# Optimization experiments

Hardware: AMD Instinct MI355X
Metric: run time of the kernel (lower is better)

Reference implementation:

```python
import jax, jax.numpy as jnp
import numpy as np

HEADS = 16
DIM_HEAD = 64
LN_EPS = 1e-5


def setup_inputs() -> dict:
    key = jax.random.key(0)
    ks = jax.random.split(key, 4)
    b, n, dim = 2, 2048, 1024
    inner = HEADS * DIM_HEAD
    x = jax.random.normal(ks[0], (b, n, dim), dtype=jnp.float32)
    gamma = jnp.ones((dim,), dtype=jnp.float32)
    beta = jnp.zeros((dim,), dtype=jnp.float32)
    w_qkv = jax.random.normal(ks[1], (dim, 3 * inner), dtype=jnp.float32) * (dim ** -0.5)
    w_out = jax.random.normal(ks[2], (inner, dim), dtype=jnp.float32) * (inner ** -0.5)
    b_out = jnp.zeros((dim,), dtype=jnp.float32)
    return {"x": x, "gamma": gamma, "beta": beta, "w_qkv": w_qkv, "w_out": w_out, "b_out": b_out}


def reference(x, gamma, beta, w_qkv, w_out, b_out):
    b, n, dim = x.shape
    h, d = HEADS, DIM_HEAD
    scale = d ** -0.5
    # LayerNorm
    mu = jnp.mean(x, axis=-1, keepdims=True)
    var = jnp.mean(jnp.square(x - mu), axis=-1, keepdims=True)
    xn = (x - mu) * jax.lax.rsqrt(var + LN_EPS) * gamma + beta
    # QKV projection (no bias)
    qkv = xn @ w_qkv  # [b, n, 3*h*d]
    q, k, v = jnp.split(qkv, 3, axis=-1)
    split_heads = lambda t: t.reshape(b, n, h, d).transpose(0, 2, 1, 3)  # [b, h, n, d]
    q, k, v = split_heads(q), split_heads(k), split_heads(v)
    q = q * scale
    sim = jnp.einsum('bhid,bhjd->bhij', q, k)  # full O(n^2) score matrix
    attn = jax.nn.softmax(sim, axis=-1)
    out = jnp.einsum('bhij,bhjd->bhid', attn, v)
    out = out.transpose(0, 2, 1, 3).reshape(b, n, h * d)
    return out @ w_out + b_out
```

## Files before the change

kernel.cpp:

```cpp
#include <hip/hip_runtime.h>
#include <hip/hip_bf16.h>

#define HEADS 16
#define DH 64
#define DIM 1024
#define SEQ 2048
#define BATCH 2
#define ROWS (BATCH*SEQ)
#define NQKV (3*DIM)
#define NKVT (SEQ/64)
#define NSPLIT 2
#define QSCALE 0.18033688011112042f
#define NBH (BATCH*HEADS)
#define NQROWS (NBH*SEQ)

typedef __attribute__((ext_vector_type(8))) short bf16x8;
typedef __attribute__((ext_vector_type(4))) float f32x4;
typedef __attribute__((ext_vector_type(16))) float f32x16;
typedef __attribute__((ext_vector_type(4))) unsigned u32x4;
typedef __hip_bfloat16 bf16;

static __device__ __forceinline__ bf16 f2bf(float v){ return __float2bfloat16(v); }

static __device__ __forceinline__ unsigned cvtpk(float a, float b){
  unsigned r;
  asm("v_cvt_pk_bf16_f32 %0, %1, %2" : "=v"(r) : "v"(a), "v"(b));
  return r;
}

static __device__ __forceinline__ void gload16(const void* g, void* lds){
  __builtin_amdgcn_global_load_lds((const __attribute__((address_space(1))) void*)g,
                                   (__attribute__((address_space(3))) void*)lds, 16, 0, 0);
}

__global__ __launch_bounds__(256) void ln_kernel(const float* __restrict__ x,
    const float* __restrict__ gamma, const float* __restrict__ beta,
    bf16* __restrict__ xn)
{
  int row = blockIdx.x;
  int tid = threadIdx.x;
  float4 v = ((const float4*)(x + (size_t)row*DIM))[tid];
  float s  = v.x+v.y+v.z+v.w;
  float ss = v.x*v.x+v.y*v.y+v.z*v.z+v.w*v.w;
  #pragma unroll
  for (int m=1;m<64;m<<=1){ s += __shfl_xor(s,m); ss += __shfl_xor(ss,m); }
  __shared__ float red[8];
  int wid = tid>>6;
  if ((tid&63)==0){ red[wid]=s; red[4+wid]=ss; }
  __syncthreads();
  s  = red[0]+red[1]+red[2]+red[3];
  ss = red[4]+red[5]+red[6]+red[7];
  float mu  = s*(1.0f/DIM);
  float var = ss*(1.0f/DIM) - mu*mu;
  float inv = rsqrtf(var + 1e-5f);
  float4 g  = ((const float4*)gamma)[tid];
  float4 bb = ((const float4*)beta)[tid];
  __align__(8) bf16 o[4];
  o[0]=f2bf((v.x-mu)*inv*g.x+bb.x);
  o[1]=f2bf((v.y-mu)*inv*g.y+bb.y);
  o[2]=f2bf((v.z-mu)*inv*g.z+bb.z);
  o[3]=f2bf((v.w-mu)*inv*g.w+bb.w);
  *(uint2*)&xn[(size_t)row*DIM + tid*4] = *(const uint2*)o;
}

__global__ __launch_bounds__(256) void transpose_cast(const float* __restrict__ in,
    bf16* __restrict__ out, int R, int C)
{
  __shared__ __align__(16) bf16 t[64][72];
  int c0 = blockIdx.x*64, r0 = blockIdx.y*64;
  int tid = threadIdx.x;
  int row = tid>>2;
  int cq  = (tid&3)*16;
  #pragma unroll
  for (int j=0;j<4;j++){
    float4 v = *(const float4*)&in[(size_t)(r0+row)*C + c0 + cq + j*4];
    t[cq+j*4+0][row] = f2bf(v.x);
    t[cq+j*4+1][row] = f2bf(v.y);
    t[cq+j*4+2][row] = f2bf(v.z);
    t[cq+j*4+3][row] = f2bf(v.w);
  }
  __syncthreads();
  int c = tid>>2; int rq = (tid&3)*16;
  uint4 u0 = *(const uint4*)&t[c][rq];
  uint4 u1 = *(const uint4*)&t[c][rq+8];
  *(uint4*)&out[(size_t)(c0+c)*R + r0 + rq]     = u0;
  *(uint4*)&out[(size_t)(c0+c)*R + r0 + rq + 8] = u1;
}

template<int BM>
__global__ __launch_bounds__(256) void gemm_bt(
    const bf16* __restrict__ A, const bf16* __restrict__ Bt, int K, int mode,
    bf16* __restrict__ qb, bf16* __restrict__ kb, bf16* __restrict__ vtb,
    float* __restrict__ outf, const float* __restrict__ bias)
{
  constexpr int MT = (BM == 128) ? 4 : 2;
  __shared__ __align__(16) bf16 aL[2][BM*32];
  __shared__ __align__(16) bf16 bL[2][128*32];
  int tid = threadIdx.x;
  int w = tid>>6, l = tid&63;
  int lr = l&15, lh = l>>4;
  int wr = w>>1, wc = w&1;
  int by = blockIdx.y, bx = blockIdx.x;
  const bf16* Ab = A  + (size_t)(by*BM)*K;
  const bf16* Bb = Bt + (size_t)(bx*128)*K;
  int srow = w*32 + (l>>2);
  int scol = ((l&3)*8) ^ (((l>>2)&3)<<3);
  int frsw = (lr&3)<<3;
  int nt = K/32;

  f32x4 acc[MT][4] = {};

  auto STAGE = [&](int buf, int k0){
    if constexpr (BM == 128){
      gload16(Ab + (size_t)(srow   )*K + k0 + scol, &aL[buf][w*1024      ]);
      gload16(Ab + (size_t)(srow+16)*K + k0 + scol, &aL[buf][w*1024 + 512]);
    } else {
      gload16(Ab + (size_t)(tid>>2 )*K + k0 + scol, &aL[buf][w*512       ]);
    }
    gload16(Bb + (size_t)(srow   )*K + k0 + scol, &bL[buf][w*1024      ]);
    gload16(Bb + (size_t)(srow+16)*K + k0 + scol, &bL[buf][w*1024 + 512]);
  };

  STAGE(0, 0);
  for (int t=0; t<nt; t++){
    int cur = t&1;
    __syncthreads();
    if (t+1 < nt) STAGE(cur^1, (t+1)*32);
    bf16x8 af[MT], bfr[4];
    #pragma unroll
    for (int m=0;m<MT;m++)
      af[m]  = *(const bf16x8*)&aL[cur][(wr*(MT*16) + m*16 + lr)*32 + ((lh*8) ^ frsw)];
    #pragma unroll
    for (int n=0;n<4;n++)
      bfr[n] = *(const bf16x8*)&bL[cur][(wc*64 + n*16 + lr)*32 + ((lh*8) ^ frsw)];
    #pragma unroll
    for (int m=0;m<MT;m++)
      #pragma unroll
      for (int n=0;n<4;n++)
        acc[m][n] = __builtin_amdgcn_mfma_f32_16x16x32_bf16(af[m], bfr[n], acc[m][n], 0,0,0);
  }
  int rb = by*BM + wr*(MT*16), cb = bx*128 + wc*64;
  if (mode == 1){
    #pragma unroll
    for (int m=0;m<MT;m++)
      #pragma unroll
      for (int n=0;n<4;n++)
        #pragma unroll
        for (int reg=0;reg<4;reg++){
          int r = rb + m*16 + lh*4 + reg;
          int c = cb + n*16 + lr;
          outf[(size_t)r*DIM + c] = acc[m][n][reg] + bias[c];
        }
  } else if (bx < 8){
    int b = rb >> 11;
    int nn0 = rb & 2047;
    #pragma unroll
    for (int m=0;m<MT;m++)
      #pragma unroll
      for (int n=0;n<4;n++)
        #pragma unroll
        for (int reg=0;reg<4;reg++){
          int nn = nn0 + m*16 + lh*4 + reg;
          int c  = cb + n*16 + lr;
          int hh = c >> 6, dd = c & 63;
          qb[((size_t)(b*HEADS + hh)*SEQ + nn)*DH + dd] = f2bf(acc[m][n][reg]*QSCALE);
        }
  } else if (bx < 16){
    int b = rb >> 11;
    int kvt = (rb & 2047) >> 6;
    int hh0 = ((cb - 1024) >> 6);
    #pragma unroll
    for (int m=0;m<MT;m++)
      #pragma unroll
      for (int reg=0;reg<4;reg++){
        int kvi = m*16 + lh*4 + reg;
        int sw  = (kvi&7)<<3;
        #pragma unroll
        for (int n=0;n<4;n++){
          int dd = n*16 + lr;
          kb[((size_t)(b*HEADS + hh0)*NKVT + kvt)*4096 + kvi*64 + (dd ^ sw)] = f2bf(acc[m][n][reg]);
        }
      }
  } else {
    __syncthreads();
    bf16* tl = (w < 2 ? (bf16*)aL : (bf16*)bL) + (w&1)*4096;
    int b   = rb >> 11;
    int kvt = (rb & 2047) >> 6;
    int hh  = (cb - 2048) >> 6;
    #pragma unroll
    for (int n=0;n<4;n++){
      int dd = n*16 + lr;
      int sw = (dd&7)<<3;
      #pragma unroll
      for (int m=0;m<MT;m++)
        #pragma unroll
        for (int reg=0;reg<4;reg++)
          tl[dd*64 + ((m*16 + lh*4 + reg) ^ sw)] = f2bf(acc[m][n][reg]);
    }
    __syncthreads();
    size_t gb = ((size_t)(b*HEADS + hh)*NKVT + kvt)*4096;
    #pragma unroll
    for (int j=0;j<8;j++)
      *(uint4*)&vtb[gb + j*512 + l*8] = *(const uint4*)&tl[j*512 + l*8];
  }
}

__global__ __launch_bounds__(256,4) void attn_part(
    const bf16* __restrict__ qb, const bf16* __restrict__ kb,
    const bf16* __restrict__ vtb,
    float* __restrict__ Opart, float* __restrict__ Mpart, float* __restrict__ Spart)
{
  __shared__ __align__(16) bf16 Kl[2][4096];
  __shared__ __align__(16) bf16 Vl[2][4096];
  int tid = threadIdx.x;
  int w = tid>>6, l = tid&63;
  int q5 = l & 31;
  int hi = l >> 5;
  int swz = (q5&7)<<3;
  int bh = blockIdx.y;
  int sp = blockIdx.z;
  int ts = sp*16, te = ts+16;
  const bf16* Q  = qb  + (size_t)bh*SEQ*DH;
  const bf16* Kt = kb  + (size_t)bh*NKVT*4096;
  const bf16* Vt = vtb + (size_t)bh*NKVT*4096;
  int q0w = blockIdx.x*128 + w*32;

  int co[4];
  #pragma unroll
  for (int st=0;st<4;st++) co[st] = (st*16 + hi*8) ^ swz;
  int r0 = q5*64, r1 = r0 + 2048;

  bf16x8 qf[4];
  #pragma unroll
  for (int st=0;st<4;st++)
    qf[st] = *(const bf16x8*)&Q[(size_t)(q0w + q5)*DH + st*16 + hi*8];

  bf16x8 vone;
  #pragma unroll
  for (int i=0;i<8;i++) vone[i] = (short)0x3f80;

  f32x16 o0 = {}, o1 = {}, osum = {};
  float mrun = -3e38f;

  {
    const bf16* ks = Kt + (size_t)ts*4096;
    const bf16* vs = Vt + (size_t)ts*4096;
    gload16(ks + w*1024       + l*8, &Kl[0][w*1024      ]);
    gload16(ks + w*1024 + 512 + l*8, &Kl[0][w*1024 + 512]);
    gload16(vs + w*1024       + l*8, &Vl[0][w*1024      ]);
    gload16(vs + w*1024 + 512 + l*8, &Vl[0][w*1024 + 512]);
  }

  for (int t=ts; t<te; t++){
    int cur = (t-ts)&1;
    __syncthreads();
    if (t+1 < te){
      const bf16* ks = Kt + (size_t)(t+1)*4096;
      const bf16* vs = Vt + (size_t)(t+1)*4096;
      gload16(ks + w*1024       + l*8, &Kl[cur^1][w*1024      ]);
      gload16(ks + w*1024 + 512 + l*8, &Kl[cur^1][w*1024 + 512]);
      gload16(vs + w*1024       + l*8, &Vl[cur^1][w*1024      ]);
      gload16(vs + w*1024 + 512 + l*8, &Vl[cur^1][w*1024 + 512]);
    }
    f32x16 s0 = {}, s1 = {};
    __builtin_amdgcn_s_setprio(1);
    #pragma unroll
    for (int st=0;st<4;st++){
      bf16x8 kf0 = *(const bf16x8*)&Kl[cur][r0 + co[st]];
      bf16x8 kf1 = *(const bf16x8*)&Kl[cur][r1 + co[st]];
      s0 = __builtin_amdgcn_mfma_f32_32x32x16_bf16(kf0, qf[st], s0, 0,0,0);
      s1 = __builtin_amdgcn_mfma_f32_32x32x16_bf16(kf1, qf[st], s1, 0,0,0);
    }
    __builtin_amdgcn_s_setprio(0);
    float pm = -3e38f;
    #pragma unroll
    for (int r=0;r<16;r++) pm = fmaxf(pm, fmaxf(s0[r], s1[r]));
    pm = fmaxf(pm, __shfl_xor(pm, 32));
    if (__any(pm > mrun + 8.f)){
      float mn = fmaxf(mrun, pm);
      float sc = __builtin_amdgcn_exp2f(mrun - mn);
      mrun = mn;
      #pragma unroll
      for (int reg=0;reg<16;reg++){
        float scr = __shfl(sc, (l & 32) | ((reg&3) + 8*(reg>>2) + 4*hi));
        o0[reg] *= scr;
        o1[reg] *= scr;
        osum[reg] *= scr;
      }
    }
    #pragma unroll
    for (int r=0;r<16;r++){
      s0[r] = __builtin_amdgcn_exp2f(s0[r] - mrun);
      s1[r] = __builtin_amdgcn_exp2f(s1[r] - mrun);
    }
    #define PV_STEP(SV, SGN, KVS)                                                    \
    {                                                                                \
      unsigned Aw = cvtpk(SV[SGN+0], SV[SGN+1]);                                     \
      unsigned Bw = cvtpk(SV[SGN+2], SV[SGN+3]);                                     \
      unsigned Cw = cvtpk(SV[SGN+4], SV[SGN+5]);                                     \
      unsigned Dw = cvtpk(SV[SGN+6], SV[SGN+7]);                                     \
      asm volatile("v_permlane32_swap_b32 %0, %1" : "+v"(Aw), "+v"(Cw));             \
      asm volatile("v_permlane32_swap_b32 %0, %1" : "+v"(Bw), "+v"(Dw));             \
      u32x4 pw = {Aw, Bw, Cw, Dw};                                                   \
      bf16x8 pa = *(const bf16x8*)&pw;                                               \
      bf16x8 vf0 = *(const bf16x8*)&Vl[cur][r0 + co[KVS]];                           \
      bf16x8 vf1 = *(const bf16x8*)&Vl[cur][r1 + co[KVS]];                           \
      __builtin_amdgcn_s_setprio(1);                                                 \
      o0 = __builtin_amdgcn_mfma_f32_32x32x16_bf16(pa, vf0, o0, 0,0,0);              \
      o1 = __builtin_amdgcn_mfma_f32_32x32x16_bf16(pa, vf1, o1, 0,0,0);              \
      osum = __builtin_amdgcn_mfma_f32_32x32x16_bf16(pa, vone, osum, 0,0,0);         \
      __builtin_amdgcn_s_setprio(0);                                                 \
    }
    PV_STEP(s0, 0, 0)
    PV_STEP(s0, 8, 1)
    PV_STEP(s1, 0, 2)
    PV_STEP(s1, 8, 3)
    #undef PV_STEP
  }
  size_t rbase = ((size_t)sp*NBH + bh)*SEQ;
  #pragma unroll
  for (int reg=0;reg<16;reg++){
    int q = q0w + (reg&3) + 8*(reg>>2) + 4*hi;
    Opart[(rbase + q)*64 + q5]      = o0[reg];
    Opart[(rbase + q)*64 + 32 + q5] = o1[reg];
  }
  if (l < 32)
    Mpart[rbase + q0w + l] = mrun;
  if (q5 == 0){
    #pragma unroll
    for (int reg=0;reg<16;reg++){
      int q = q0w + (reg&3) + 8*(reg>>2) + 4*hi;
      Spart[rbase + q] = osum[reg];
    }
  }
}

__global__ __launch_bounds__(256) void attn_merge(
    const float* __restrict__ Opart, const float* __restrict__ Mpart,
    const float* __restrict__ Spart, bf16* __restrict__ ao)
{
  int r = blockIdx.x*4 + (threadIdx.x>>6);
  int d = threadIdx.x & 63;
  float m0 = Mpart[r], m1 = Mpart[NQROWS + r];
  float m  = fmaxf(m0, m1);
  float c0 = exp2f(m0 - m), c1 = exp2f(m1 - m);
  float denom = Spart[r]*c0 + Spart[NQROWS + r]*c1;
  float v = Opart[(size_t)r*64 + d]*c0
          + Opart[((size_t)NQROWS + r)*64 + d]*c1;
  int bh = r >> 11, q = r & 2047;
  int b = bh >> 4, h = bh & 15;
  ao[((size_t)(b*SEQ + q))*DIM + h*DH + d] = f2bf(v / denom);
}

extern "C" void kernel_launch(void* const* d_in, const int* in_sizes, int n_in,
                              void* d_out, int out_size, void* d_ws, size_t ws_size,
                              hipStream_t stream)
{
  const float* x     = (const float*)d_in[0];
  const float* gamma = (const float*)d_in[1];
  const float* beta  = (const float*)d_in[2];
  const float* w_qkv = (const float*)d_in[3];
  const float* w_out = (const float*)d_in[4];
  const float* b_out = (const float*)d_in[5];
  float* out = (float*)d_out;

  bf16* ws  = (bf16*)d_ws;
  bf16* xn  = ws;
  bf16* wqt = xn  + (size_t)ROWS*DIM;
  bf16* wot = wqt + (size_t)NQKV*DIM;
  bf16* qb  = wot + (size_t)DIM*DIM;
  bf16* kb  = qb  + (size_t)NBH*SEQ*DH;
  bf16* vtb = kb  + (size_t)NBH*SEQ*DH;
  bf16* ao  = vtb + (size_t)NBH*SEQ*DH;
  float* Opart = (float*)(ao + (size_t)ROWS*DIM);
  float* Mpart = Opart + (size_t)NSPLIT*NQROWS*DH;
  float* Spart = Mpart + (size_t)NSPLIT*NQROWS;

  ln_kernel<<<dim3(ROWS), dim3(256), 0, stream>>>(x, gamma, beta, xn);
  transpose_cast<<<dim3(NQKV/64, DIM/64), dim3(256), 0, stream>>>(w_qkv, wqt, DIM, NQKV);
  transpose_cast<<<dim3(DIM/64,  DIM/64), dim3(256), 0, stream>>>(w_out, wot, DIM, DIM);
  gemm_bt<128><<<dim3(NQKV/128, ROWS/128), dim3(256), 0, stream>>>(
      xn, wqt, DIM, 0, qb, kb, vtb, (float*)nullptr, (const float*)nullptr);
  attn_part<<<dim3(SEQ/128, NBH, NSPLIT), dim3(256), 0, stream>>>(
      qb, kb, vtb, Opart, Mpart, Spart);
  attn_merge<<<dim3(NQROWS/4), dim3(256), 0, stream>>>(Opart, Mpart, Spart, ao);
  gemm_bt<64><<<dim3(DIM/128, ROWS/64), dim3(256), 0, stream>>>(
      ao, wot, DIM, 1, (bf16*)nullptr, (bf16*)nullptr, (bf16*)nullptr, out, b_out);
}
```

Baseline: 133.3 us.

## Triple-buffer GEMM LDS staging and store attention partials in bf16

```diff
diff --git a/kernel.cpp b/kernel.cpp
--- a/kernel.cpp
+++ b/kernel.cpp
@@ -94,8 +94,8 @@
     float* __restrict__ outf, const float* __restrict__ bias)
 {
   constexpr int MT = (BM == 128) ? 4 : 2;
-  __shared__ __align__(16) bf16 aL[2][BM*32];
-  __shared__ __align__(16) bf16 bL[2][128*32];
+  __shared__ __align__(16) bf16 aL[3][BM*32];
+  __shared__ __align__(16) bf16 bL[3][128*32];
   int tid = threadIdx.x;
   int w = tid>>6, l = tid&63;
   int lr = l&15, lh = l>>4;
@@ -121,24 +121,39 @@
     gload16(Bb + (size_t)(srow+16)*K + k0 + scol, &bL[buf][w*1024 + 512]);
   };
 
-  STAGE(0, 0);
-  for (int t=0; t<nt; t++){
-    int cur = t&1;
-    __syncthreads();
-    if (t+1 < nt) STAGE(cur^1, (t+1)*32);
+  auto COMPUTE = [&](int buf){
     bf16x8 af[MT], bfr[4];
     #pragma unroll
     for (int m=0;m<MT;m++)
-      af[m]  = *(const bf16x8*)&aL[cur][(wr*(MT*16) + m*16 + lr)*32 + ((lh*8) ^ frsw)];
+      af[m]  = *(const bf16x8*)&aL[buf][(wr*(MT*16) + m*16 + lr)*32 + ((lh*8) ^ frsw)];
     #pragma unroll
     for (int n=0;n<4;n++)
-      bfr[n] = *(const bf16x8*)&bL[cur][(wc*64 + n*16 + lr)*32 + ((lh*8) ^ frsw)];
+      bfr[n] = *(const bf16x8*)&bL[buf][(wc*64 + n*16 + lr)*32 + ((lh*8) ^ frsw)];
     #pragma unroll
     for (int m=0;m<MT;m++)
       #pragma unroll
       for (int n=0;n<4;n++)
         acc[m][n] = __builtin_amdgcn_mfma_f32_16x16x32_bf16(af[m], bfr[n], acc[m][n], 0,0,0);
-  }
+  };
+
+  STAGE(0, 0);
+  STAGE(1, 32);
+  int cur = 0;
+  for (int t=0; t<nt-1; t++){
+    if constexpr (BM == 128) asm volatile("s_waitcnt vmcnt(4)" ::: "memory");
+    else                     asm volatile("s_waitcnt vmcnt(3)" ::: "memory");
+    __builtin_amdgcn_s_barrier();
+    __builtin_amdgcn_sched_barrier(0);
+    int s2 = cur + 2; if (s2 >= 3) s2 -= 3;
+    if (t+2 < nt) STAGE(s2, (t+2)*32);
+    COMPUTE(cur);
+    cur = (cur == 2) ? 0 : cur + 1;
+  }
+  asm volatile("s_waitcnt vmcnt(0)" ::: "memory");
+  __builtin_amdgcn_s_barrier();
+  __builtin_amdgcn_sched_barrier(0);
+  COMPUTE(cur);
+
   int rb = by*BM + wr*(MT*16), cb = bx*128 + wc*64;
   if (mode == 1){
     #pragma unroll
@@ -208,7 +223,7 @@
 __global__ __launch_bounds__(256,4) void attn_part(
     const bf16* __restrict__ qb, const bf16* __restrict__ kb,
     const bf16* __restrict__ vtb,
-    float* __restrict__ Opart, float* __restrict__ Mpart, float* __restrict__ Spart)
+    bf16* __restrict__ Opart, float* __restrict__ Mpart, float* __restrict__ Spart)
 {
   __shared__ __align__(16) bf16 Kl[2][4096];
   __shared__ __align__(16) bf16 Vl[2][4096];
@@ -321,8 +336,8 @@
   #pragma unroll
   for (int reg=0;reg<16;reg++){
     int q = q0w + (reg&3) + 8*(reg>>2) + 4*hi;
-    Opart[(rbase + q)*64 + q5]      = o0[reg];
-    Opart[(rbase + q)*64 + 32 + q5] = o1[reg];
+    Opart[(rbase + q)*64 + q5]      = f2bf(o0[reg]);
+    Opart[(rbase + q)*64 + 32 + q5] = f2bf(o1[reg]);
   }
   if (l < 32)
     Mpart[rbase + q0w + l] = mrun;
@@ -336,7 +351,7 @@
 }
 
 __global__ __launch_bounds__(256) void attn_merge(
-    const float* __restrict__ Opart, const float* __restrict__ Mpart,
+    const bf16* __restrict__ Opart, const float* __restrict__ Mpart,
     const float* __restrict__ Spart, bf16* __restrict__ ao)
 {
   int r = blockIdx.x*4 + (threadIdx.x>>6);
@@ -345,8 +360,8 @@
   float m  = fmaxf(m0, m1);
   float c0 = exp2f(m0 - m), c1 = exp2f(m1 - m);
   float denom = Spart[r]*c0 + Spart[NQROWS + r]*c1;
-  float v = Opart[(size_t)r*64 + d]*c0
-          + Opart[((size_t)NQROWS + r)*64 + d]*c1;
+  float v = __bfloat162float(Opart[(size_t)r*64 + d])*c0
+          + __bfloat162float(Opart[((size_t)NQROWS + r)*64 + d])*c1;
   int bh = r >> 11, q = r & 2047;
   int b = bh >> 4, h = bh & 15;
   ao[((size_t)(b*SEQ + q))*DIM + h*DH + d] = f2bf(v / denom);
@@ -372,8 +387,8 @@
   bf16* kb  = qb  + (size_t)NBH*SEQ*DH;
   bf16* vtb = kb  + (size_t)NBH*SEQ*DH;
   bf16* ao  = vtb + (size_t)NBH*SEQ*DH;
-  float* Opart = (float*)(ao + (size_t)ROWS*DIM);
-  float* Mpart = Opart + (size_t)NSPLIT*NQROWS*DH;
+  bf16* Opart = ao + (size_t)ROWS*DIM;
+  float* Mpart = (float*)(Opart + (size_t)NSPLIT*NQROWS*DH);
   float* Spart = Mpart + (size_t)NSPLIT*NQROWS;
 
   ln_kernel<<<dim3(ROWS), dim3(256), 0, stream>>>(x, gamma, beta, xn);
```

Result: no change. 130.8 us (-1.9%).
